# Optimization experiments

Hardware: AMD Instinct MI355X
Metric: run time of the kernel (lower is better)

## Reference

```python
import jax, jax.numpy as jnp
import numpy as np

B, N, D = 8, 1024, 768
H, HD = 12, 64


def setup_inputs() -> dict:
    key = jax.random.key(0)
    ks = jax.random.split(key, 9)
    return {
        "x": jax.random.normal(ks[0], (B, N, D), dtype=jnp.float32),
        "Wq": jax.random.normal(ks[1], (H, HD, HD), dtype=jnp.float32) * (HD ** -0.5),
        "Wk": jax.random.normal(ks[2], (H, HD, HD), dtype=jnp.float32) * (HD ** -0.5),
        "Wv": jax.random.normal(ks[3], (H, HD, HD), dtype=jnp.float32) * (HD ** -0.5),
        "bq": jax.random.normal(ks[4], (H, HD), dtype=jnp.float32) * 0.02,
        "bk": jax.random.normal(ks[5], (H, HD), dtype=jnp.float32) * 0.02,
        "bv": jax.random.normal(ks[6], (H, HD), dtype=jnp.float32) * 0.02,
        "Wo": jax.random.normal(ks[7], (D, D), dtype=jnp.float32) * (D ** -0.5),
        "bo": jnp.zeros((D,), dtype=jnp.float32),
    }


def reference(x, Wq, Wk, Wv, bq, bk, bv, Wo, bo):
    # x: [B, N, D]; split into H heads of size HD along the feature dim
    b, n, d = x.shape
    h, hd = Wq.shape[0], Wq.shape[1]
    xh = x.reshape(b, n, h, hd)
    # per-head linear projections (stacked nn.Linear(head_dim, head_dim))
    q = jnp.einsum('bnhd,hde->bhne', xh, Wq) + bq[None, :, None, :]
    k = jnp.einsum('bnhd,hde->bhne', xh, Wk) + bk[None, :, None, :]
    v = jnp.einsum('bnhd,hde->bhne', xh, Wv) + bv[None, :, None, :]
    # NOTE: faithful quirk - scale uses FULL dim, not head_dim
    scale = d ** -0.5
    scores = jnp.einsum('bhid,bhjd->bhij', q, k) * scale  # [B,H,N,N]
    attn = jax.nn.softmax(scores, axis=-1)
    out = jnp.einsum('bhij,bhjd->bhid', attn, v)  # [B,H,N,HD]
    out = out.transpose(0, 2, 1, 3).reshape(b, n, d)  # concat heads
    return out @ Wo.T + bo  # wO: nn.Linear(dim, dim)
```

## Files before the change

### kernel.cpp

```cpp
#include <hip/hip_runtime.h>


typedef __attribute__((ext_vector_type(8))) short short8;
typedef __attribute__((ext_vector_type(4))) float floatx4;

#define MFMA16(a, b, c) __builtin_amdgcn_mfma_f32_16x16x32_bf16((a), (b), (c), 0, 0, 0)

#if __has_builtin(__builtin_amdgcn_exp2f)
#define EXP2(x) __builtin_amdgcn_exp2f(x)
#else
#define EXP2(x) __expf(0.6931471805599453f * (x))
#endif
#if __has_builtin(__builtin_amdgcn_rcpf)
#define RCP(x) __builtin_amdgcn_rcpf(x)
#else
#define RCP(x) (1.0f / (x))
#endif

__device__ __forceinline__ unsigned short f2bf(float f) {
    union { float f; unsigned int i; } c;
    c.f = f;
    unsigned int i = c.i;
    return (unsigned short)((i + 0x7fffu + ((i >> 16) & 1u)) >> 16);
}
__device__ __forceinline__ unsigned short f2bf_trunc(float f) {
    union { float f; unsigned int i; } c;
    c.f = f;
    return (unsigned short)(c.i >> 16);
}

__global__ __launch_bounds__(256) void prep_weights(
    const float* __restrict__ Wq, const float* __restrict__ Wk,
    const float* __restrict__ Wv, const float* __restrict__ Wo,
    unsigned short* __restrict__ Wqt, unsigned short* __restrict__ Wkt,
    unsigned short* __restrict__ Wvt, unsigned short* __restrict__ Wob)
{
    int tid = blockIdx.x * 256 + threadIdx.x;
    if (tid < 49152) {
        int h = tid >> 12, r = tid & 4095;
        int e = r >> 6, k = r & 63;
        int src = h * 4096 + k * 64 + e, dst = h * 4096 + e * 64 + k;
        Wqt[dst] = f2bf(Wq[src]);
        Wkt[dst] = f2bf(Wk[src]);
        Wvt[dst] = f2bf(Wv[src]);
    }
    for (int i = tid; i < 589824; i += 147456) Wob[i] = f2bf(Wo[i]);
}

__global__ __launch_bounds__(256) void qkv_proj(
    const float* __restrict__ x,
    const unsigned short* __restrict__ Wqt, const unsigned short* __restrict__ Wkt,
    const unsigned short* __restrict__ Wvt,
    const float* __restrict__ bq, const float* __restrict__ bk,
    const float* __restrict__ bv,
    unsigned short* __restrict__ Q, unsigned short* __restrict__ K,
    unsigned short* __restrict__ Vt)
{
    __shared__ __align__(16) unsigned short xlds[64 * 72];
    __shared__ __align__(16) unsigned short vlds[64 * 72];

    const int bh = blockIdx.y;
    const int b = bh / 12, h = bh % 12;
    const int wave = threadIdx.x >> 6, lane = threadIdx.x & 63;
    const int lrow = lane & 15, quad = lane >> 4;
    const int row0 = blockIdx.x * 64;
    const float scale = 0.052058776672f;

    {
        const int tr = threadIdx.x >> 2;
        const int tc = threadIdx.x & 3;
        const float* src = x + ((size_t)(b * 1024 + row0 + tr)) * 768
                           + h * 64 + tc * 16;
        float4 f0 = *(const float4*)(src);
        float4 f1 = *(const float4*)(src + 4);
        float4 f2 = *(const float4*)(src + 8);
        float4 f3 = *(const float4*)(src + 12);
        short8 p0, p1;
        p0[0] = (short)f2bf(f0.x); p0[1] = (short)f2bf(f0.y);
        p0[2] = (short)f2bf(f0.z); p0[3] = (short)f2bf(f0.w);
        p0[4] = (short)f2bf(f1.x); p0[5] = (short)f2bf(f1.y);
        p0[6] = (short)f2bf(f1.z); p0[7] = (short)f2bf(f1.w);
        p1[0] = (short)f2bf(f2.x); p1[1] = (short)f2bf(f2.y);
        p1[2] = (short)f2bf(f2.z); p1[3] = (short)f2bf(f2.w);
        p1[4] = (short)f2bf(f3.x); p1[5] = (short)f2bf(f3.y);
        p1[6] = (short)f2bf(f3.z); p1[7] = (short)f2bf(f3.w);
        *(short8*)&xlds[tr * 72 + tc * 16] = p0;
        *(short8*)&xlds[tr * 72 + tc * 16 + 8] = p1;
    }
    __syncthreads();

    short8 xb0 = *(const short8*)&xlds[(wave * 16 + lrow) * 72 + quad * 8];
    short8 xb1 = *(const short8*)&xlds[(wave * 16 + lrow) * 72 + 32 + quad * 8];

    const floatx4 zero = { 0.f, 0.f, 0.f, 0.f };

    const unsigned short* Wm[2] = { Wqt + h * 4096, Wkt + h * 4096 };
    const float* bm[2] = { bq + h * 64, bk + h * 64 };
    unsigned short* Om[2] = {
        Q + ((size_t)bh * 1024 + row0 + wave * 16 + lrow) * 64,
        K + ((size_t)bh * 1024 + row0 + wave * 16 + lrow) * 64 };
    #pragma unroll
    for (int m = 0; m < 2; ++m) {
        const unsigned short* W = Wm[m];
        #pragma unroll
        for (int t = 0; t < 4; ++t) {
            short8 wa0 = *(const short8*)(W + (t * 16 + lrow) * 64 + quad * 8);
            short8 wa1 = *(const short8*)(W + (t * 16 + lrow) * 64 + 32 + quad * 8);
            floatx4 acc = zero;
            acc = MFMA16(wa0, xb0, acc);
            acc = MFMA16(wa1, xb1, acc);
            float4 bias = *(const float4*)(bm[m] + t * 16 + quad * 4);
            const float bs[4] = { bias.x, bias.y, bias.z, bias.w };
            unsigned short pkd[4];
            #pragma unroll
            for (int r = 0; r < 4; ++r) {
                float v = acc[r] + bs[r];
                if (m == 0) v *= scale;
                pkd[r] = f2bf(v);
            }
            *(uint2*)(Om[m] + t * 16 + quad * 4) = *(uint2*)pkd;
        }
    }

    {
        const unsigned short* W = Wvt + h * 4096;
        const float* bvh = bv + h * 64;
        #pragma unroll
        for (int t = 0; t < 4; ++t) {
            short8 wa0 = *(const short8*)(W + (t * 16 + lrow) * 64 + quad * 8);
            short8 wa1 = *(const short8*)(W + (t * 16 + lrow) * 64 + 32 + quad * 8);
            floatx4 acc = zero;
            acc = MFMA16(wa0, xb0, acc);
            acc = MFMA16(wa1, xb1, acc);
            float4 bias = *(const float4*)(bvh + t * 16 + quad * 4);
            const float bs[4] = { bias.x, bias.y, bias.z, bias.w };
            #pragma unroll
            for (int r = 0; r < 4; ++r)
                vlds[(t * 16 + quad * 4 + r) * 72 + wave * 16 + lrow]
                    = f2bf(acc[r] + bs[r]);
        }
    }
    __syncthreads();
    {
        const int er = threadIdx.x >> 2;
        const int sc = threadIdx.x & 3;
        short8 v0 = *(const short8*)&vlds[er * 72 + sc * 16];
        short8 v1 = *(const short8*)&vlds[er * 72 + sc * 16 + 8];
        unsigned short* dst = Vt + (size_t)bh * 65536 + (size_t)er * 1024
                              + row0 + sc * 16;
        *(short8*)dst = v0;
        *(short8*)(dst + 8) = v1;
    }
}

__global__ __launch_bounds__(256) void attn_kernel(
    const unsigned short* __restrict__ Q, const unsigned short* __restrict__ K,
    const unsigned short* __restrict__ Vt, unsigned short* __restrict__ AO)
{
    __shared__ __align__(16) unsigned short Klds[64 * 72];
    __shared__ __align__(16) unsigned short Vlds[64 * 72];

    const int bh = (int)blockIdx.x + ((int)blockIdx.y >> 3) * 8;
    const int qb = blockIdx.y & 7;
    const int b = bh / 12, h = bh % 12;
    const int wave = threadIdx.x >> 6, lane = threadIdx.x & 63;
    const int lrow = lane & 15, quad = lane >> 4;
    const int qrow0 = qb * 128 + wave * 32;

    const unsigned short* Qb = Q + (size_t)bh * 65536;
    const unsigned short* Kb = K + (size_t)bh * 65536;
    const unsigned short* Vb = Vt + (size_t)bh * 65536;

    const int tch = threadIdx.x & 7, trow = threadIdx.x >> 3;
    const int slot0 = ((trow & 4) << 2) | ((trow >> 3) << 2) | (trow & 3);

    short8 aq[2][2];
    #pragma unroll
    for (int mm = 0; mm < 2; ++mm) {
        const unsigned short* qr = Qb + (size_t)(qrow0 + mm * 16 + lrow) * 64;
        aq[mm][0] = *(const short8*)(qr + quad * 8);
        aq[mm][1] = *(const short8*)(qr + 32 + quad * 8);
    }

    const floatx4 zero = { 0.f, 0.f, 0.f, 0.f };
    float part[2] = { 0.f, 0.f };
    floatx4 Oacc[2][4];
    #pragma unroll
    for (int mm = 0; mm < 2; ++mm)
        #pragma unroll
        for (int t = 0; t < 4; ++t) Oacc[mm][t] = zero;

    short8 kpre[2], vpre[2];
    kpre[0] = *(const short8*)(Kb + (size_t)trow * 64 + tch * 8);
    kpre[1] = *(const short8*)(Kb + (size_t)(trow + 32) * 64 + tch * 8);
    vpre[0] = *(const short8*)(Vb + (size_t)trow * 1024 + tch * 8);
    vpre[1] = *(const short8*)(Vb + (size_t)(trow + 32) * 1024 + tch * 8);

    for (int jt = 0; jt < 16; ++jt) {
        *(short8*)&Klds[slot0 * 72 + tch * 8] = kpre[0];
        *(short8*)&Klds[(slot0 + 32) * 72 + tch * 8] = kpre[1];
        *(short8*)&Vlds[trow * 72 + tch * 8] = vpre[0];
        *(short8*)&Vlds[(trow + 32) * 72 + tch * 8] = vpre[1];
        __syncthreads();

        {
            const int jn = ((jt + 1) & 15) * 64;
            kpre[0] = *(const short8*)(Kb + (size_t)(jn + trow) * 64 + tch * 8);
            kpre[1] = *(const short8*)(Kb + (size_t)(jn + trow + 32) * 64 + tch * 8);
            vpre[0] = *(const short8*)(Vb + (size_t)trow * 1024 + jn + tch * 8);
            vpre[1] = *(const short8*)(Vb + (size_t)(trow + 32) * 1024 + jn + tch * 8);
        }

        #pragma unroll
        for (int w = 0; w < 2; ++w) {
            short8 kA[2][2];
            #pragma unroll
            for (int tau = 0; tau < 2; ++tau) {
                int kr = w * 32 + tau * 16 + lrow;
                kA[tau][0] = *(const short8*)&Klds[kr * 72 + quad * 8];
                kA[tau][1] = *(const short8*)&Klds[kr * 72 + 32 + quad * 8];
            }
            short8 vA[4];
            #pragma unroll
            for (int t = 0; t < 4; ++t)
                vA[t] = *(const short8*)&Vlds[(t * 16 + lrow) * 72
                                              + w * 32 + quad * 8];

            #pragma unroll
            for (int mm = 0; mm < 2; ++mm) {
                floatx4 s0 = zero, s1 = zero;
                s0 = MFMA16(kA[0][0], aq[mm][0], s0);
                s0 = MFMA16(kA[0][1], aq[mm][1], s0);
                s1 = MFMA16(kA[1][0], aq[mm][0], s1);
                s1 = MFMA16(kA[1][1], aq[mm][1], s1);

                short8 pk;
                #pragma unroll
                for (int r = 0; r < 4; ++r) {
                    float p0 = EXP2(s0[r]);
                    float p1 = EXP2(s1[r]);
                    part[mm] += p0 + p1;
                    pk[r] = (short)f2bf_trunc(p0);
                    pk[4 + r] = (short)f2bf_trunc(p1);
                }
                #pragma unroll
                for (int t = 0; t < 4; ++t)
                    Oacc[mm][t] = MFMA16(vA[t], pk, Oacc[mm][t]);
            }
        }
        __syncthreads();
    }

    #pragma unroll
    for (int mm = 0; mm < 2; ++mm) {
        float ts = part[mm];
        ts += __shfl_xor(ts, 16);
        ts += __shfl_xor(ts, 32);
        float inv = RCP(ts);
        unsigned short* orow = AO
            + ((size_t)(b * 1024 + qrow0 + mm * 16 + lrow)) * 768 + h * 64;
        #pragma unroll
        for (int t = 0; t < 4; ++t) {
            unsigned short pkd[4];
            #pragma unroll
            for (int r = 0; r < 4; ++r)
                pkd[r] = f2bf(Oacc[mm][t][r] * inv);
            *(uint2*)(orow + t * 16 + quad * 4) = *(uint2*)pkd;
        }
    }
}

__global__ __launch_bounds__(256) void out_proj(
    const unsigned short* __restrict__ AO, const unsigned short* __restrict__ Wob,
    const float* __restrict__ bo, float* __restrict__ Y)
{
    __shared__ __align__(16) unsigned short Alds[128 * 40];
    __shared__ __align__(16) unsigned short Blds[64 * 40];

    const int wave = threadIdx.x >> 6, lane = threadIdx.x & 63;
    const int lrow = lane & 15, quad = lane >> 4;
    const int row0 = blockIdx.x * 128;
    const int c0 = blockIdx.y * 64;
    const int wrow = (wave >> 1) * 64, wcol = (wave & 1) * 32;

    const int tch = threadIdx.x & 3, trow = threadIdx.x >> 2;

    const floatx4 zero = { 0.f, 0.f, 0.f, 0.f };
    floatx4 acc[2][4];
    #pragma unroll
    for (int u = 0; u < 2; ++u)
        #pragma unroll
        for (int t = 0; t < 4; ++t) acc[u][t] = zero;

    for (int k0 = 0; k0 < 768; k0 += 32) {
        #pragma unroll
        for (int rr = 0; rr < 2; ++rr) {
            int r = trow + rr * 64;
            *(short8*)&Alds[r * 40 + tch * 8] =
                *(const short8*)(AO + (size_t)(row0 + r) * 768 + k0 + tch * 8);
        }
        *(short8*)&Blds[trow * 40 + tch * 8] =
            *(const short8*)(Wob + (size_t)(c0 + trow) * 768 + k0 + tch * 8);
        __syncthreads();

        short8 aoF[4], wF[2];
        #pragma unroll
        for (int t = 0; t < 4; ++t)
            aoF[t] = *(const short8*)&Alds[(wrow + t * 16 + lrow) * 40 + quad * 8];
        #pragma unroll
        for (int u = 0; u < 2; ++u)
            wF[u] = *(const short8*)&Blds[(wcol + u * 16 + lrow) * 40 + quad * 8];

        #pragma unroll
        for (int u = 0; u < 2; ++u)
            #pragma unroll
            for (int t = 0; t < 4; ++t)
                acc[u][t] = MFMA16(wF[u], aoF[t], acc[u][t]);
        __syncthreads();
    }

    #pragma unroll
    for (int u = 0; u < 2; ++u) {
        const int cb = c0 + wcol + u * 16 + quad * 4;
        float4 bias = *(const float4*)(bo + cb);
        const float bs[4] = { bias.x, bias.y, bias.z, bias.w };
        #pragma unroll
        for (int t = 0; t < 4; ++t) {
            const int row = row0 + wrow + t * 16 + lrow;
            float out[4];
            #pragma unroll
            for (int r = 0; r < 4; ++r) out[r] = acc[u][t][r] + bs[r];
            *(float4*)(Y + (size_t)row * 768 + cb) = *(float4*)out;
        }
    }
}

extern "C" void kernel_launch(void* const* d_in, const int* in_sizes, int n_in,
                              void* d_out, int out_size, void* d_ws, size_t ws_size,
                              hipStream_t stream)
{
    const float* x  = (const float*)d_in[0];
    const float* Wq = (const float*)d_in[1];
    const float* Wk = (const float*)d_in[2];
    const float* Wv = (const float*)d_in[3];
    const float* bq = (const float*)d_in[4];
    const float* bk = (const float*)d_in[5];
    const float* bv = (const float*)d_in[6];
    const float* Wo = (const float*)d_in[7];
    const float* bo = (const float*)d_in[8];

    unsigned short* Q   = (unsigned short*)d_ws;
    unsigned short* K   = Q + 6291456;
    unsigned short* Vt  = K + 6291456;
    unsigned short* AO  = Vt + 6291456;
    unsigned short* Wqt = AO + 6291456;
    unsigned short* Wkt = Wqt + 49152;
    unsigned short* Wvt = Wkt + 49152;
    unsigned short* Wob = Wvt + 49152;
    float* Y = (float*)d_out;

    prep_weights<<<dim3(576), 256, 0, stream>>>(Wq, Wk, Wv, Wo, Wqt, Wkt, Wvt, Wob);
    qkv_proj<<<dim3(16, 96), 256, 0, stream>>>(x, Wqt, Wkt, Wvt, bq, bk, bv, Q, K, Vt);
    attn_kernel<<<dim3(8, 96), 256, 0, stream>>>(Q, K, Vt, AO);
    out_proj<<<dim3(64, 12), 256, 0, stream>>>(AO, Wob, bo, Y);
}
```

Before: 173.4 us.

## Prefetch out_proj tiles into registers with deeper K step; coalesce x load

The output projection GEMM now uses a 64-wide K tile instead of 32 and software-pipelines global loads: the next tile is fetched into registers while MFMAs run on the current LDS tile. This halves the number of barrier pairs and hides global load latency, at the cost of more registers and more LDS. The QKV kernel's x load is also reorganized so that 16 consecutive threads read one 64-float row segment as float4s, which gives more coalesced global reads.

```diff
diff --git a/kernel.cpp b/kernel.cpp
--- a/kernel.cpp
+++ b/kernel.cpp
@@ -67,25 +67,19 @@
     const float scale = 0.052058776672f;
 
     {
-        const int tr = threadIdx.x >> 2;
-        const int tc = threadIdx.x & 3;
-        const float* src = x + ((size_t)(b * 1024 + row0 + tr)) * 768
-                           + h * 64 + tc * 16;
-        float4 f0 = *(const float4*)(src);
-        float4 f1 = *(const float4*)(src + 4);
-        float4 f2 = *(const float4*)(src + 8);
-        float4 f3 = *(const float4*)(src + 12);
-        short8 p0, p1;
-        p0[0] = (short)f2bf(f0.x); p0[1] = (short)f2bf(f0.y);
-        p0[2] = (short)f2bf(f0.z); p0[3] = (short)f2bf(f0.w);
-        p0[4] = (short)f2bf(f1.x); p0[5] = (short)f2bf(f1.y);
-        p0[6] = (short)f2bf(f1.z); p0[7] = (short)f2bf(f1.w);
-        p1[0] = (short)f2bf(f2.x); p1[1] = (short)f2bf(f2.y);
-        p1[2] = (short)f2bf(f2.z); p1[3] = (short)f2bf(f2.w);
-        p1[4] = (short)f2bf(f3.x); p1[5] = (short)f2bf(f3.y);
-        p1[6] = (short)f2bf(f3.z); p1[7] = (short)f2bf(f3.w);
-        *(short8*)&xlds[tr * 72 + tc * 16] = p0;
-        *(short8*)&xlds[tr * 72 + tc * 16 + 8] = p1;
+        const int tr = threadIdx.x >> 4;
+        const int tc = (threadIdx.x & 15) * 4;
+        #pragma unroll
+        for (int rr = 0; rr < 4; ++rr) {
+            const int r = tr + rr * 16;
+            const float* src = x + ((size_t)(b * 1024 + row0 + r)) * 768
+                               + h * 64 + tc;
+            float4 f = *(const float4*)src;
+            unsigned short pkd[4];
+            pkd[0] = f2bf(f.x); pkd[1] = f2bf(f.y);
+            pkd[2] = f2bf(f.z); pkd[3] = f2bf(f.w);
+            *(uint2*)&xlds[r * 72 + tc] = *(uint2*)pkd;
+        }
     }
     __syncthreads();
 
@@ -274,8 +268,8 @@
     const unsigned short* __restrict__ AO, const unsigned short* __restrict__ Wob,
     const float* __restrict__ bo, float* __restrict__ Y)
 {
-    __shared__ __align__(16) unsigned short Alds[128 * 40];
-    __shared__ __align__(16) unsigned short Blds[64 * 40];
+    __shared__ __align__(16) unsigned short Alds[128 * 72];
+    __shared__ __align__(16) unsigned short Blds[64 * 72];
 
     const int wave = threadIdx.x >> 6, lane = threadIdx.x & 63;
     const int lrow = lane & 15, quad = lane >> 4;
@@ -283,7 +277,7 @@
     const int c0 = blockIdx.y * 64;
     const int wrow = (wave >> 1) * 64, wcol = (wave & 1) * 32;
 
-    const int tch = threadIdx.x & 3, trow = threadIdx.x >> 2;
+    const int tch = threadIdx.x & 7, trow = threadIdx.x >> 3;
 
     const floatx4 zero = { 0.f, 0.f, 0.f, 0.f };
     floatx4 acc[2][4];
@@ -292,30 +286,54 @@
         #pragma unroll
         for (int t = 0; t < 4; ++t) acc[u][t] = zero;
 
-    for (int k0 = 0; k0 < 768; k0 += 32) {
-        #pragma unroll
-        for (int rr = 0; rr < 2; ++rr) {
-            int r = trow + rr * 64;
-            *(short8*)&Alds[r * 40 + tch * 8] =
-                *(const short8*)(AO + (size_t)(row0 + r) * 768 + k0 + tch * 8);
-        }
-        *(short8*)&Blds[trow * 40 + tch * 8] =
-            *(const short8*)(Wob + (size_t)(c0 + trow) * 768 + k0 + tch * 8);
+    short8 apre[4], bpre[2];
+    #pragma unroll
+    for (int rr = 0; rr < 4; ++rr)
+        apre[rr] = *(const short8*)(AO + (size_t)(row0 + trow + rr * 32) * 768
+                                    + tch * 8);
+    #pragma unroll
+    for (int rr = 0; rr < 2; ++rr)
+        bpre[rr] = *(const short8*)(Wob + (size_t)(c0 + trow + rr * 32) * 768
+                                    + tch * 8);
+
+    for (int k0 = 0; k0 < 768; k0 += 64) {
+        #pragma unroll
+        for (int rr = 0; rr < 4; ++rr)
+            *(short8*)&Alds[(trow + rr * 32) * 72 + tch * 8] = apre[rr];
+        #pragma unroll
+        for (int rr = 0; rr < 2; ++rr)
+            *(short8*)&Blds[(trow + rr * 32) * 72 + tch * 8] = bpre[rr];
         __syncthreads();
 
-        short8 aoF[4], wF[2];
-        #pragma unroll
-        for (int t = 0; t < 4; ++t)
-            aoF[t] = *(const short8*)&Alds[(wrow + t * 16 + lrow) * 40 + quad * 8];
-        #pragma unroll
-        for (int u = 0; u < 2; ++u)
-            wF[u] = *(const short8*)&Blds[(wcol + u * 16 + lrow) * 40 + quad * 8];
-
-        #pragma unroll
-        for (int u = 0; u < 2; ++u)
+        {
+            const int kn = (k0 + 64 < 768) ? k0 + 64 : 0;
+            #pragma unroll
+            for (int rr = 0; rr < 4; ++rr)
+                apre[rr] = *(const short8*)(AO
+                    + (size_t)(row0 + trow + rr * 32) * 768 + kn + tch * 8);
+            #pragma unroll
+            for (int rr = 0; rr < 2; ++rr)
+                bpre[rr] = *(const short8*)(Wob
+                    + (size_t)(c0 + trow + rr * 32) * 768 + kn + tch * 8);
+        }
+
+        #pragma unroll
+        for (int kc = 0; kc < 2; ++kc) {
+            short8 aoF[4], wF[2];
             #pragma unroll
             for (int t = 0; t < 4; ++t)
-                acc[u][t] = MFMA16(wF[u], aoF[t], acc[u][t]);
+                aoF[t] = *(const short8*)&Alds[(wrow + t * 16 + lrow) * 72
+                                               + kc * 32 + quad * 8];
+            #pragma unroll
+            for (int u = 0; u < 2; ++u)
+                wF[u] = *(const short8*)&Blds[(wcol + u * 16 + lrow) * 72
+                                              + kc * 32 + quad * 8];
+            #pragma unroll
+            for (int u = 0; u < 2; ++u)
+                #pragma unroll
+                for (int t = 0; t < 4; ++t)
+                    acc[u][t] = MFMA16(wF[u], aoF[t], acc[u][t]);
+        }
         __syncthreads();
     }
 
```

After: 169.6 us. 1.02x faster.
